# Performance work log

Hardware: AMD Instinct MI355X
Metric: run time of the kernel (lower is better)

## Reference

```python
import jax, jax.numpy as jnp
import numpy as np

BLOCK_SIZE = 64


def setup_inputs() -> dict:
    key = jax.random.key(0)
    kq, kk, kv, km = jax.random.split(key, 4)
    H, N, D = 16, 8192, 64
    nb = N // BLOCK_SIZE
    return {
        "q": jax.random.normal(kq, (H, N, D), dtype=jnp.float32),
        "k": jax.random.normal(kk, (H, N, D), dtype=jnp.float32),
        "v": jax.random.normal(kv, (H, N, D), dtype=jnp.float32),
        "block_mask": jax.random.randint(km, (nb, nb), 0, 2, dtype=jnp.int32),
    }


def reference(q, k, v, block_mask):
    """Block-sparse flash attention with online softmax.

    q, k, v: [H, N, D]; block_mask: [N//B, N//B] (1 = valid, 0 = masked).
    Scans over key blocks, processing all query rows at once; masked blocks
    contribute exactly zero (exp(-inf) = 0), matching the original's skip.
    """
    H, N, D = q.shape
    B = BLOCK_SIZE
    nb = N // B
    scale = D ** -0.5

    kb = k.reshape(H, nb, B, D).transpose(1, 0, 2, 3)  # [nb, H, B, D]
    vb = v.reshape(H, nb, B, D).transpose(1, 0, 2, 3)  # [nb, H, B, D]
    mask_cols = block_mask.T  # [nb_key, nb_query]: row j = validity of key block j per query block

    m0 = jnp.full((H, N, 1), -jnp.inf, dtype=q.dtype)
    l0 = jnp.zeros((H, N, 1), dtype=q.dtype)
    o0 = jnp.zeros((H, N, D), dtype=q.dtype)

    def step(carry, xs):
        m, l, o = carry
        k_j, v_j, mcol = xs  # k_j/v_j: [H, B, D]; mcol: [nb] over query blocks
        logits = jnp.einsum('hnd,hbd->hnb', q, k_j) * scale  # [H, N, B]
        valid = (jnp.repeat(mcol, B) > 0)[None, :, None]      # [1, N, 1]
        logits = jnp.where(valid, logits, -jnp.inf)
        m_new = jnp.maximum(m, logits.max(-1, keepdims=True))
        # guard: if everything so far is masked, m_new = -inf; use 0 to keep exps finite (=0)
        m_safe = jnp.where(jnp.isneginf(m_new), jnp.zeros_like(m_new), m_new)
        a_old = jnp.exp(m - m_safe)       # rescale of previous accumulators
        p = jnp.exp(logits - m_safe)      # masked entries -> 0
        l = a_old * l + p.sum(-1, keepdims=True)
        o = a_old * o + jnp.einsum('hnb,hbd->hnd', p, v_j)
        return (m_new, l, o), None

    (m, l, o), _ = jax.lax.scan(step, (m0, l0, o0), (kb, vb, mask_cols))
    return o / l
```

## Files before the change

kernel.cpp:

```cpp
#include <hip/hip_runtime.h>

#define Hh 16
#define Nn 8192
#define Dd 64
#define NB 128

typedef float  f32x4   __attribute__((ext_vector_type(4)));
typedef float  f32x16  __attribute__((ext_vector_type(16)));
typedef float  float4_ __attribute__((ext_vector_type(4)));
typedef short  bf16x8  __attribute__((ext_vector_type(8)));
typedef unsigned short ushort8  __attribute__((ext_vector_type(8)));
typedef unsigned short ushort4_ __attribute__((ext_vector_type(4)));

typedef const __attribute__((address_space(1))) unsigned int gu32;
typedef __attribute__((address_space(3))) unsigned int lu32;

#define QSCALE 0.1803368801111244f

__device__ __forceinline__ unsigned short f2bf(float f) {
    union { float f; unsigned u; } x; x.f = f;
    unsigned r = x.u + 0x7fffu + ((x.u >> 16) & 1u);
    return (unsigned short)(r >> 16);
}

__device__ __forceinline__ unsigned pack2bf(float lo, float hi) {
    return (unsigned)f2bf(lo) | ((unsigned)f2bf(hi) << 16);
}

__global__ void cvt_k(const float* __restrict__ k, unsigned short* __restrict__ ko) {
    int i = blockIdx.x * 256 + threadIdx.x;
    float4_ b = ((const float4_*)k)[i];
    ushort4_ ob;
#pragma unroll
    for (int j = 0; j < 4; ++j) ob[j] = f2bf(b[j]);
    ((ushort4_*)ko)[i] = ob;
}

__global__ void cvt_vt(const float* __restrict__ v, unsigned short* __restrict__ vt) {
    int jb = blockIdx.x, h = blockIdx.y, t = threadIdx.x;
    __shared__ float T[64][65];
    const float4_* src = (const float4_*)(v + ((long)h * Nn + jb * 64) * Dd);
#pragma unroll
    for (int it = 0; it < 4; ++it) {
        int r = (t >> 4) + it * 16;
        int c0 = (t & 15) * 4;
        float4_ x = src[r * 16 + (t & 15)];
#pragma unroll
        for (int i2 = 0; i2 < 4; ++i2) T[c0 + i2][r] = x[i2];
    }
    __syncthreads();
    int d = t >> 2, seg = (t & 3) * 16;
    ushort8 o0, o1;
#pragma unroll
    for (int i2 = 0; i2 < 8; ++i2) o0[i2] = f2bf(T[d][seg + i2]);
#pragma unroll
    for (int i2 = 0; i2 < 8; ++i2) o1[i2] = f2bf(T[d][seg + 8 + i2]);
    unsigned short* dst = vt + ((long)h * Dd + d) * Nn + jb * 64 + seg;
    *(ushort8*)dst = o0;
    *(ushort8*)(dst + 8) = o1;
}

__global__ __launch_bounds__(128, 2) void attn32(
        const unsigned short* __restrict__ k16,
        const unsigned short* __restrict__ vt16,
        const float* __restrict__ qf,
        const int* __restrict__ mask,
        float* __restrict__ out) {
    int bid = blockIdx.x;
    int h = (bid & 7) | ((bid >> 10) << 3);
    int qb = (bid >> 3) & 127;
    int tid = threadIdx.x;
    int wid = tid >> 6, l = tid & 63;
    int q5 = l & 31, hi = l >> 5;

    __shared__ unsigned short Kl[2][4096];
    __shared__ unsigned short Vl[2][4096];

    const int* mrow = mask + qb * NB;
    unsigned long long b0 = __ballot(mrow[l] != 0);
    unsigned long long b1 = __ballot(mrow[64 + l] != 0);
    int count = __popcll(b0) + __popcll(b1);

    if (count == 0) {
        float4_ z = {0.f, 0.f, 0.f, 0.f};
        float4_* ob = (float4_*)(out + ((size_t)h * Nn + qb * 64) * Dd);
        for (int x = tid; x < 64 * 64 / 4; x += 128) ob[x] = z;
        return;
    }

    size_t qrow = (size_t)h * Nn + qb * 64 + wid * 32 + q5;
    bf16x8 qfrag[4];
#pragma unroll
    for (int ds_ = 0; ds_ < 4; ++ds_) {
        const float4_* qs = (const float4_*)(qf + qrow * Dd + ds_ * 16 + hi * 8);
        float4_ x = qs[0], y = qs[1];
        union { unsigned short s[8]; bf16x8 v; } u;
#pragma unroll
        for (int i2 = 0; i2 < 4; ++i2) {
            u.s[i2]     = f2bf(x[i2] * QSCALE);
            u.s[4 + i2] = f2bf(y[i2] * QSCALE);
        }
        qfrag[ds_] = u.v;
    }

    const unsigned short* sp[8];
    int jmul;
    if (wid == 0) {
        jmul = 64 * Dd;
#pragma unroll
        for (int f = 0; f < 8; ++f)
            sp[f] = k16 + (size_t)h * (Nn * Dd)
                  + (size_t)(q5 + 32 * (f >> 2)) * Dd + (f & 3) * 16 + hi * 8;
    } else {
        jmul = 64;
#pragma unroll
        for (int f = 0; f < 8; ++f)
            sp[f] = vt16 + (size_t)h * (Nn * Dd)
                  + (size_t)(q5 + 32 * (f >> 2)) * Nn + (f & 3) * 16 + hi * 8;
    }

    unsigned long long r0 = b0, r1 = b1;
    auto next_j = [&]() {
        int jj;
        if (r0) { jj = __ffsll(r0) - 1; r0 &= r0 - 1; }
        else    { jj = 63 + __ffsll(r1); r1 &= r1 - 1; }
        return jj;
    };

    auto issue = [&](int nbuf, int jj) {
        unsigned short* lb = (wid == 0) ? &Kl[nbuf][0] : &Vl[nbuf][0];
#pragma unroll
        for (int f = 0; f < 8; ++f) {
            const unsigned short* g = sp[f] + (size_t)jj * jmul;
            __builtin_amdgcn_global_load_lds((gu32*)g, (lu32*)(lb + f * 512), 16, 0, 0);
        }
    };

    issue(0, next_j());

    f32x16 o0 = {}, o1 = {};
    float l_run = 0.f;

    for (int i = 0; i < count; ++i) {
        int buf = i & 1;
        __syncthreads();
        if (i + 1 < count) issue(buf ^ 1, next_j());

        const char* kb = (const char*)Kl + buf * 8192 + l * 16;
        const char* vb = (const char*)Vl + buf * 8192 + l * 16;

        f32x16 s0 = {}, s1 = {};
#pragma unroll
        for (int ds_ = 0; ds_ < 4; ++ds_) {
            bf16x8 kf0 = *(const bf16x8*)(kb + ds_ * 1024);
            s0 = __builtin_amdgcn_mfma_f32_32x32x16_bf16(kf0, qfrag[ds_], s0, 0, 0, 0);
        }
#pragma unroll
        for (int ds_ = 0; ds_ < 4; ++ds_) {
            bf16x8 kf1 = *(const bf16x8*)(kb + 4096 + ds_ * 1024);
            s1 = __builtin_amdgcn_mfma_f32_32x32x16_bf16(kf1, qfrag[ds_], s1, 0, 0, 0);
        }

#pragma unroll
        for (int e = 0; e < 16; ++e) s0[e] = __builtin_amdgcn_exp2f(s0[e]);
#pragma unroll
        for (int e = 0; e < 16; ++e) s1[e] = __builtin_amdgcn_exp2f(s1[e]);

        float sr[8];
#pragma unroll
        for (int e = 0; e < 8; ++e) sr[e] = (s0[e] + s0[e + 8]) + (s1[e] + s1[e + 8]);
#pragma unroll
        for (int e = 0; e < 4; ++e) sr[e] += sr[e + 4];
        float ps = (sr[0] + sr[1]) + (sr[2] + sr[3]);
        ps += __shfl_xor(ps, 32);
        l_run += ps;

        unsigned w0[8], w1[8];
#pragma unroll
        for (int jj = 0; jj < 8; ++jj) {
            w0[jj] = pack2bf(s0[2 * jj], s0[2 * jj + 1]);
            w1[jj] = pack2bf(s1[2 * jj], s1[2 * jj + 1]);
        }
        auto swap32 = [&](unsigned& a, unsigned& b) {
            unsigned send = hi ? a : b;
            unsigned recv = (unsigned)__shfl_xor((int)send, 32);
            a = hi ? recv : a;
            b = hi ? b : recv;
        };
        swap32(w0[0], w0[2]); swap32(w0[1], w0[3]);
        swap32(w0[4], w0[6]); swap32(w0[5], w0[7]);
        swap32(w1[0], w1[2]); swap32(w1[1], w1[3]);
        swap32(w1[4], w1[6]); swap32(w1[5], w1[7]);

        union U { unsigned u[4]; bf16x8 v; };
        U pbs[4];
        pbs[0].u[0] = w0[0]; pbs[0].u[1] = w0[1]; pbs[0].u[2] = w0[2]; pbs[0].u[3] = w0[3];
        pbs[1].u[0] = w0[4]; pbs[1].u[1] = w0[5]; pbs[1].u[2] = w0[6]; pbs[1].u[3] = w0[7];
        pbs[2].u[0] = w1[0]; pbs[2].u[1] = w1[1]; pbs[2].u[2] = w1[2]; pbs[2].u[3] = w1[3];
        pbs[3].u[0] = w1[4]; pbs[3].u[1] = w1[5]; pbs[3].u[2] = w1[6]; pbs[3].u[3] = w1[7];

#pragma unroll
        for (int c = 0; c < 4; ++c) {
            bf16x8 vf0 = *(const bf16x8*)(vb + c * 1024);
            o0 = __builtin_amdgcn_mfma_f32_32x32x16_bf16(vf0, pbs[c].v, o0, 0, 0, 0);
        }
#pragma unroll
        for (int c = 0; c < 4; ++c) {
            bf16x8 vf1 = *(const bf16x8*)(vb + 4096 + c * 1024);
            o1 = __builtin_amdgcn_mfma_f32_32x32x16_bf16(vf1, pbs[c].v, o1, 0, 0, 0);
        }
    }

    float inv = 1.0f / l_run;
    float* obase = out + ((size_t)h * Nn + qb * 64 + wid * 32 + q5) * Dd;
#pragma unroll
    for (int s4 = 0; s4 < 4; ++s4) {
        float4_ t0, t1;
#pragma unroll
        for (int e = 0; e < 4; ++e) { t0[e] = o0[4 * s4 + e] * inv; t1[e] = o1[4 * s4 + e] * inv; }
        *(float4_*)(obase + 8 * s4 + 4 * hi)      = t0;
        *(float4_*)(obase + 32 + 8 * s4 + 4 * hi) = t1;
    }
}

__global__ void attn_main(const float* __restrict__ qf, const float* __restrict__ kf,
                          const float* __restrict__ vf, const int* __restrict__ mask,
                          float* __restrict__ out) {
    int id = blockIdx.x;
    int h = id & 15, qb = id >> 4;
    int tid = threadIdx.x;
    int lane = tid & 63, wid = tid >> 6;
    int l15 = lane & 15, l4 = lane >> 4;

    __shared__ unsigned short Kl[2][64 * 64];
    __shared__ unsigned short Vl[2][64 * 64];
    __shared__ unsigned short Pl[4][16 * 64];

    const int* mrow = mask + qb * NB;
    unsigned long long b0 = __ballot(mrow[lane] != 0);
    unsigned long long b1 = __ballot(mrow[64 + lane] != 0);
    int count = __popcll(b0) + __popcll(b1);

    float* op = out + ((long)h * Nn + qb * 64 + wid * 16) * Dd;

    if (count == 0) {
#pragma unroll
        for (int r = 0; r < 4; ++r)
#pragma unroll
            for (int dn = 0; dn < 4; ++dn)
                op[(l4 * 4 + r) * Dd + dn * 16 + l15] = 0.f;
        return;
    }

    long qrow = (long)h * Nn + qb * 64 + wid * 16 + l15;
    bf16x8 qfrag[2];
#pragma unroll
    for (int dc = 0; dc < 2; ++dc) {
        const float4_* qs = (const float4_*)qf + qrow * 16 + dc * 8 + l4 * 2;
        float4_ x = qs[0], y = qs[1];
        union { unsigned short s[8]; bf16x8 v; } u;
#pragma unroll
        for (int i2 = 0; i2 < 4; ++i2) {
            u.s[i2] = f2bf(x[i2] * 0.125f);
            u.s[4 + i2] = f2bf(y[i2] * 0.125f);
        }
        qfrag[dc] = u.v;
    }

    int sgq = tid & 7;
    int srow = tid >> 3;
    float4_ kf4[2][2]; float4_ vf4[4];
    int vk = tid & 63, vd0 = (tid >> 6) * 16;

    auto load_kv = [&](int j) {
        const float4_* ks = (const float4_*)kf + ((long)h * Nn + j * 64) * 16;
#pragma unroll
        for (int it = 0; it < 2; ++it) {
            kf4[it][0] = ks[(srow + it * 32) * 16 + sgq * 2];
            kf4[it][1] = ks[(srow + it * 32) * 16 + sgq * 2 + 1];
        }
        const float4_* vs = (const float4_*)vf + ((long)h * Nn + j * 64) * 16;
#pragma unroll
        for (int c = 0; c < 4; ++c) vf4[c] = vs[vk * 16 + (vd0 >> 2) + c];
    };

    auto write_kv = [&](int buf) {
#pragma unroll
        for (int it = 0; it < 2; ++it) {
            int r = srow + it * 32;
            union { unsigned short s[8]; ushort8 v; } u;
#pragma unroll
            for (int i2 = 0; i2 < 4; ++i2) {
                u.s[i2] = f2bf(kf4[it][0][i2]);
                u.s[4 + i2] = f2bf(kf4[it][1][i2]);
            }
            *(ushort8*)((char*)&Kl[buf][0] + r * 128 + (((sgq ^ r) & 7) << 4)) = u.v;
        }
#pragma unroll
        for (int i2 = 0; i2 < 16; ++i2) {
            int d = vd0 + i2;
            *((unsigned short*)((char*)&Vl[buf][0] + d * 128 +
                ((((vk >> 3) ^ d) & 7) << 4) + ((vk & 7) << 1))) = f2bf(vf4[i2 >> 2][i2 & 3]);
        }
    };

    f32x4 o_acc[4] = {};
    float m_r[4], l_r[4];
#pragma unroll
    for (int r = 0; r < 4; ++r) { m_r[r] = -INFINITY; l_r[r] = 0.f; }

    unsigned long long r0 = b0, r1 = b1;
    auto next_j = [&]() {
        int jj;
        if (r0) { jj = __ffsll(r0) - 1; r0 &= r0 - 1; }
        else    { jj = 63 + __ffsll(r1); r1 &= r1 - 1; }
        return jj;
    };

    load_kv(next_j());

    for (int i = 0; i < count; ++i) {
        int buf = i & 1;
        write_kv(buf);
        __syncthreads();
        if (i + 1 < count) load_kv(next_j());

        f32x4 s[4] = {};
#pragma unroll
        for (int dc = 0; dc < 2; ++dc) {
#pragma unroll
            for (int kn = 0; kn < 4; ++kn) {
                int krow = kn * 16 + l15;
                bf16x8 kfr = *(const bf16x8*)((const char*)&Kl[buf][0] +
                               krow * 128 + ((((l4 + dc * 4) ^ krow) & 7) << 4));
                s[kn] = __builtin_amdgcn_mfma_f32_16x16x32_bf16(qfrag[dc], kfr, s[kn], 0, 0, 0);
            }
        }

#pragma unroll
        for (int r = 0; r < 4; ++r) {
            float mx = fmaxf(fmaxf(s[0][r], s[1][r]), fmaxf(s[2][r], s[3][r]));
#pragma unroll
            for (int off = 1; off < 16; off <<= 1) mx = fmaxf(mx, __shfl_xor(mx, off));
            float mn = fmaxf(m_r[r], mx);
            float a = __expf(m_r[r] - mn);
            m_r[r] = mn;
            float psum = 0.f;
#pragma unroll
            for (int kn = 0; kn < 4; ++kn) { float p = __expf(s[kn][r] - mn); s[kn][r] = p; psum += p; }
#pragma unroll
            for (int off = 1; off < 16; off <<= 1) psum += __shfl_xor(psum, off);
            l_r[r] = l_r[r] * a + psum;
            o_acc[0][r] *= a; o_acc[1][r] *= a; o_acc[2][r] *= a; o_acc[3][r] *= a;
        }

#pragma unroll
        for (int kn = 0; kn < 4; ++kn) {
#pragma unroll
            for (int r = 0; r < 4; ++r) {
                int prow = l4 * 4 + r;
                int pc = kn * 16 + l15;
                *((unsigned short*)((char*)&Pl[wid][0] + prow * 128 +
                    ((((pc >> 3) ^ prow) & 7) << 4) + ((pc & 7) << 1))) = f2bf(s[kn][r]);
            }
        }

        bf16x8 pa[2];
#pragma unroll
        for (int kc = 0; kc < 2; ++kc)
            pa[kc] = *(const bf16x8*)((const char*)&Pl[wid][0] +
                      l15 * 128 + ((((l4 + kc * 4) ^ l15) & 7) << 4));
#pragma unroll
        for (int dn = 0; dn < 4; ++dn) {
            int vrow = dn * 16 + l15;
#pragma unroll
            for (int kc = 0; kc < 2; ++kc) {
                bf16x8 vbf = *(const bf16x8*)((const char*)&Vl[buf][0] +
                             vrow * 128 + ((((l4 + kc * 4) ^ vrow) & 7) << 4));
                o_acc[dn] = __builtin_amdgcn_mfma_f32_16x16x32_bf16(pa[kc], vbf, o_acc[dn], 0, 0, 0);
            }
        }
    }

#pragma unroll
    for (int r = 0; r < 4; ++r) {
        float inv = 1.0f / l_r[r];
#pragma unroll
        for (int dn = 0; dn < 4; ++dn)
            op[(l4 * 4 + r) * Dd + dn * 16 + l15] = o_acc[dn][r] * inv;
    }
}

extern "C" void kernel_launch(void* const* d_in, const int* in_sizes, int n_in,
                              void* d_out, int out_size, void* d_ws, size_t ws_size,
                              hipStream_t stream) {
    const float* q = (const float*)d_in[0];
    const float* k = (const float*)d_in[1];
    const float* v = (const float*)d_in[2];
    const int* mask = (const int*)d_in[3];
    float* out = (float*)d_out;

    size_t elems = (size_t)Hh * Nn * Dd;
    size_t need = 2 * elems * sizeof(unsigned short);
    if (ws_size >= need) {
        unsigned short* k16 = (unsigned short*)d_ws;
        unsigned short* vt16 = k16 + elems;
        cvt_k<<<dim3((unsigned)(elems / 1024)), 256, 0, stream>>>(k, k16);
        cvt_vt<<<dim3(NB, Hh), 256, 0, stream>>>(v, vt16);
        attn32<<<dim3(Hh * NB), 128, 0, stream>>>(k16, vt16, q, mask, out);
    } else {
        attn_main<<<dim3(Hh * NB), 256, 0, stream>>>(q, k, v, mask, out);
    }
}
```

Before: 329.2 us.

## Split key block across wave pairs in attn32 and combine partial outputs via LDS

The attention kernel moves from 2 to 4 waves per block. Each pair of waves handles one 32-key half of every key block for the same 32 query rows, so each wave issues half the QK and PV MFMAs per iteration. The row-sum of probabilities is now computed with an MFMA against a ones vector instead of VALU adds and a shuffle. Partial outputs and sums from the second key-half wave are combined through shared memory at the end. This doubles the waves that can hide latency, at the cost of an extra reduction step, more LDS use and a higher launch-bounds occupancy target.

Result: slower. 341.4 us (+3.7%).

```diff
diff --git a/kernel.cpp b/kernel.cpp
--- a/kernel.cpp
+++ b/kernel.cpp
@@ -60,7 +60,7 @@
     *(ushort8*)(dst + 8) = o1;
 }
 
-__global__ __launch_bounds__(128, 2) void attn32(
+__global__ __launch_bounds__(256, 4) void attn32(
         const unsigned short* __restrict__ k16,
         const unsigned short* __restrict__ vt16,
         const float* __restrict__ qf,
@@ -72,9 +72,12 @@
     int tid = threadIdx.x;
     int wid = tid >> 6, l = tid & 63;
     int q5 = l & 31, hi = l >> 5;
-
-    __shared__ unsigned short Kl[2][4096];
-    __shared__ unsigned short Vl[2][4096];
+    int qh = wid & 1;
+    int kh = wid >> 1;
+    int stage_kv = wid >> 1;
+    int stage_half = wid & 1;
+
+    __shared__ __align__(16) char smem[32768];
 
     const int* mrow = mask + qb * NB;
     unsigned long long b0 = __ballot(mrow[l] != 0);
@@ -84,11 +87,11 @@
     if (count == 0) {
         float4_ z = {0.f, 0.f, 0.f, 0.f};
         float4_* ob = (float4_*)(out + ((size_t)h * Nn + qb * 64) * Dd);
-        for (int x = tid; x < 64 * 64 / 4; x += 128) ob[x] = z;
+        for (int x = tid; x < 64 * 64 / 4; x += 256) ob[x] = z;
         return;
     }
 
-    size_t qrow = (size_t)h * Nn + qb * 64 + wid * 32 + q5;
+    size_t qrow = (size_t)h * Nn + qb * 64 + qh * 32 + q5;
     bf16x8 qfrag[4];
 #pragma unroll
     for (int ds_ = 0; ds_ < 4; ++ds_) {
@@ -103,21 +106,23 @@
         qfrag[ds_] = u.v;
     }
 
-    const unsigned short* sp[8];
-    int jmul;
-    if (wid == 0) {
-        jmul = 64 * Dd;
-#pragma unroll
-        for (int f = 0; f < 8; ++f)
-            sp[f] = k16 + (size_t)h * (Nn * Dd)
-                  + (size_t)(q5 + 32 * (f >> 2)) * Dd + (f & 3) * 16 + hi * 8;
-    } else {
-        jmul = 64;
-#pragma unroll
-        for (int f = 0; f < 8; ++f)
-            sp[f] = vt16 + (size_t)h * (Nn * Dd)
-                  + (size_t)(q5 + 32 * (f >> 2)) * Nn + (f & 3) * 16 + hi * 8;
-    }
+    union { unsigned short s[8]; bf16x8 v; } ones;
+#pragma unroll
+    for (int i2 = 0; i2 < 8; ++i2) ones.s[i2] = 0x3F80;
+
+    const unsigned short* sp[4];
+    size_t jmul;
+#pragma unroll
+    for (int ff = 0; ff < 4; ++ff) {
+        int f = stage_half * 4 + ff;
+        if (stage_kv == 0)
+            sp[ff] = k16 + (size_t)h * (Nn * Dd)
+                   + (size_t)(q5 + 32 * (f >> 2)) * Dd + (f & 3) * 16 + hi * 8;
+        else
+            sp[ff] = vt16 + (size_t)h * (Nn * Dd)
+                   + (size_t)(q5 + 32 * (f >> 2)) * Nn + (f & 3) * 16 + hi * 8;
+    }
+    jmul = (stage_kv == 0) ? (size_t)(64 * Dd) : (size_t)64;
 
     unsigned long long r0 = b0, r1 = b1;
     auto next_j = [&]() {
@@ -128,98 +133,93 @@
     };
 
     auto issue = [&](int nbuf, int jj) {
-        unsigned short* lb = (wid == 0) ? &Kl[nbuf][0] : &Vl[nbuf][0];
-#pragma unroll
-        for (int f = 0; f < 8; ++f) {
-            const unsigned short* g = sp[f] + (size_t)jj * jmul;
-            __builtin_amdgcn_global_load_lds((gu32*)g, (lu32*)(lb + f * 512), 16, 0, 0);
+        char* base = smem + (stage_kv ? 16384 : 0) + nbuf * 8192;
+#pragma unroll
+        for (int ff = 0; ff < 4; ++ff) {
+            const unsigned short* g = sp[ff] + (size_t)jj * jmul;
+            __builtin_amdgcn_global_load_lds((gu32*)g,
+                (lu32*)(base + (stage_half * 4 + ff) * 1024), 16, 0, 0);
         }
     };
 
     issue(0, next_j());
 
-    f32x16 o0 = {}, o1 = {};
-    float l_run = 0.f;
+    f32x16 o0 = {}, o1 = {}, ls = {};
 
     for (int i = 0; i < count; ++i) {
         int buf = i & 1;
         __syncthreads();
         if (i + 1 < count) issue(buf ^ 1, next_j());
 
-        const char* kb = (const char*)Kl + buf * 8192 + l * 16;
-        const char* vb = (const char*)Vl + buf * 8192 + l * 16;
-
-        f32x16 s0 = {}, s1 = {};
+        const char* kb = smem + buf * 8192 + kh * 4096 + l * 16;
+        const char* vb = smem + 16384 + buf * 8192 + l * 16;
+
+        f32x16 s = {};
 #pragma unroll
         for (int ds_ = 0; ds_ < 4; ++ds_) {
-            bf16x8 kf0 = *(const bf16x8*)(kb + ds_ * 1024);
-            s0 = __builtin_amdgcn_mfma_f32_32x32x16_bf16(kf0, qfrag[ds_], s0, 0, 0, 0);
-        }
-#pragma unroll
-        for (int ds_ = 0; ds_ < 4; ++ds_) {
-            bf16x8 kf1 = *(const bf16x8*)(kb + 4096 + ds_ * 1024);
-            s1 = __builtin_amdgcn_mfma_f32_32x32x16_bf16(kf1, qfrag[ds_], s1, 0, 0, 0);
-        }
-
-#pragma unroll
-        for (int e = 0; e < 16; ++e) s0[e] = __builtin_amdgcn_exp2f(s0[e]);
-#pragma unroll
-        for (int e = 0; e < 16; ++e) s1[e] = __builtin_amdgcn_exp2f(s1[e]);
-
-        float sr[8];
-#pragma unroll
-        for (int e = 0; e < 8; ++e) sr[e] = (s0[e] + s0[e + 8]) + (s1[e] + s1[e + 8]);
-#pragma unroll
-        for (int e = 0; e < 4; ++e) sr[e] += sr[e + 4];
-        float ps = (sr[0] + sr[1]) + (sr[2] + sr[3]);
-        ps += __shfl_xor(ps, 32);
-        l_run += ps;
-
-        unsigned w0[8], w1[8];
-#pragma unroll
-        for (int jj = 0; jj < 8; ++jj) {
-            w0[jj] = pack2bf(s0[2 * jj], s0[2 * jj + 1]);
-            w1[jj] = pack2bf(s1[2 * jj], s1[2 * jj + 1]);
-        }
+            bf16x8 kf = *(const bf16x8*)(kb + ds_ * 1024);
+            s = __builtin_amdgcn_mfma_f32_32x32x16_bf16(kf, qfrag[ds_], s, 0, 0, 0);
+        }
+
+#pragma unroll
+        for (int e = 0; e < 16; ++e) s[e] = __builtin_amdgcn_exp2f(s[e]);
+
+        unsigned w[8];
+#pragma unroll
+        for (int jj = 0; jj < 8; ++jj) w[jj] = pack2bf(s[2 * jj], s[2 * jj + 1]);
         auto swap32 = [&](unsigned& a, unsigned& b) {
             unsigned send = hi ? a : b;
             unsigned recv = (unsigned)__shfl_xor((int)send, 32);
             a = hi ? recv : a;
             b = hi ? b : recv;
         };
-        swap32(w0[0], w0[2]); swap32(w0[1], w0[3]);
-        swap32(w0[4], w0[6]); swap32(w0[5], w0[7]);
-        swap32(w1[0], w1[2]); swap32(w1[1], w1[3]);
-        swap32(w1[4], w1[6]); swap32(w1[5], w1[7]);
+        swap32(w[0], w[2]); swap32(w[1], w[3]);
+        swap32(w[4], w[6]); swap32(w[5], w[7]);
 
         union U { unsigned u[4]; bf16x8 v; };
-        U pbs[4];
-        pbs[0].u[0] = w0[0]; pbs[0].u[1] = w0[1]; pbs[0].u[2] = w0[2]; pbs[0].u[3] = w0[3];
-        pbs[1].u[0] = w0[4]; pbs[1].u[1] = w0[5]; pbs[1].u[2] = w0[6]; pbs[1].u[3] = w0[7];
-        pbs[2].u[0] = w1[0]; pbs[2].u[1] = w1[1]; pbs[2].u[2] = w1[2]; pbs[2].u[3] = w1[3];
-        pbs[3].u[0] = w1[4]; pbs[3].u[1] = w1[5]; pbs[3].u[2] = w1[6]; pbs[3].u[3] = w1[7];
-
-#pragma unroll
-        for (int c = 0; c < 4; ++c) {
-            bf16x8 vf0 = *(const bf16x8*)(vb + c * 1024);
-            o0 = __builtin_amdgcn_mfma_f32_32x32x16_bf16(vf0, pbs[c].v, o0, 0, 0, 0);
-        }
-#pragma unroll
-        for (int c = 0; c < 4; ++c) {
-            bf16x8 vf1 = *(const bf16x8*)(vb + 4096 + c * 1024);
-            o1 = __builtin_amdgcn_mfma_f32_32x32x16_bf16(vf1, pbs[c].v, o1, 0, 0, 0);
-        }
-    }
-
-    float inv = 1.0f / l_run;
-    float* obase = out + ((size_t)h * Nn + qb * 64 + wid * 32 + q5) * Dd;
-#pragma unroll
-    for (int s4 = 0; s4 < 4; ++s4) {
-        float4_ t0, t1;
-#pragma unroll
-        for (int e = 0; e < 4; ++e) { t0[e] = o0[4 * s4 + e] * inv; t1[e] = o1[4 * s4 + e] * inv; }
-        *(float4_*)(obase + 8 * s4 + 4 * hi)      = t0;
-        *(float4_*)(obase + 32 + 8 * s4 + 4 * hi) = t1;
+        U pbs[2];
+        pbs[0].u[0] = w[0]; pbs[0].u[1] = w[1]; pbs[0].u[2] = w[2]; pbs[0].u[3] = w[3];
+        pbs[1].u[0] = w[4]; pbs[1].u[1] = w[5]; pbs[1].u[2] = w[6]; pbs[1].u[3] = w[7];
+
+        int c0 = kh * 2;
+#pragma unroll
+        for (int sl = 0; sl < 2; ++sl) {
+            bf16x8 vf0 = *(const bf16x8*)(vb + (c0 + sl) * 1024);
+            o0 = __builtin_amdgcn_mfma_f32_32x32x16_bf16(vf0, pbs[sl].v, o0, 0, 0, 0);
+        }
+#pragma unroll
+        for (int sl = 0; sl < 2; ++sl) {
+            bf16x8 vf1 = *(const bf16x8*)(vb + 4096 + (c0 + sl) * 1024);
+            o1 = __builtin_amdgcn_mfma_f32_32x32x16_bf16(vf1, pbs[sl].v, o1, 0, 0, 0);
+        }
+        ls = __builtin_amdgcn_mfma_f32_32x32x16_bf16(ones.v, pbs[0].v, ls, 0, 0, 0);
+        ls = __builtin_amdgcn_mfma_f32_32x32x16_bf16(ones.v, pbs[1].v, ls, 0, 0, 0);
+    }
+
+    __syncthreads();
+    float* comb = (float*)smem;
+    if (kh == 1) {
+        float* dst = comb + (qh * 64 + l) * 33;
+#pragma unroll
+        for (int e = 0; e < 16; ++e) { dst[e] = o0[e]; dst[16 + e] = o1[e]; }
+        dst[32] = ls[0];
+    }
+    __syncthreads();
+    if (kh == 0) {
+        const float* src = comb + (qh * 64 + l) * 33;
+#pragma unroll
+        for (int e = 0; e < 16; ++e) { o0[e] += src[e]; o1[e] += src[16 + e]; }
+        float inv = 1.0f / (ls[0] + src[32]);
+
+        float* obase = out + qrow * Dd;
+#pragma unroll
+        for (int s4 = 0; s4 < 4; ++s4) {
+            float4_ t0, t1;
+#pragma unroll
+            for (int e = 0; e < 4; ++e) { t0[e] = o0[4 * s4 + e] * inv; t1[e] = o1[4 * s4 + e] * inv; }
+            *(float4_*)(obase + 8 * s4 + 4 * hi)      = t0;
+            *(float4_*)(obase + 32 + 8 * s4 + 4 * hi) = t1;
+        }
     }
 }
 
@@ -407,7 +407,7 @@
         unsigned short* vt16 = k16 + elems;
         cvt_k<<<dim3((unsigned)(elems / 1024)), 256, 0, stream>>>(k, k16);
         cvt_vt<<<dim3(NB, Hh), 256, 0, stream>>>(v, vt16);
-        attn32<<<dim3(Hh * NB), 128, 0, stream>>>(k16, vt16, q, mask, out);
+        attn32<<<dim3(Hh * NB), 256, 0, stream>>>(k16, vt16, q, mask, out);
     } else {
         attn_main<<<dim3(Hh * NB), 256, 0, stream>>>(q, k, v, mask, out);
     }
```
